# Kernel optimization log

Measured on AMD Instinct MI355X. Metric: run time of the kernel, lower is better.

The kernel has to match this reference:

```python
import jax, jax.numpy as jnp
import numpy as np


def _compute_gradient(f, src, dst, egw):
    # f: [b, c, n] node features; src/dst: [b, e] edge endpoints; egw: [b, e, d]
    # gradient at node src = sum_edges pinvdx * (f[dst] - f[src])
    fT = f.transpose(0, 2, 1)  # b, n, c
    n = fT.shape[1]
    f_dst = jnp.take_along_axis(fT, dst[..., None], axis=1)  # b, e, c
    f_src = jnp.take_along_axis(fT, src[..., None], axis=1)  # b, e, c
    msg = egw[..., :, None] * (f_dst - f_src)[..., None, :]  # b, e, d, c
    b, e, d, c = msg.shape

    def seg(m, s):
        return jax.ops.segment_sum(m.reshape(e, d * c), s, num_segments=n)

    grad = jax.vmap(seg)(msg, src)  # b, n, d*c
    return grad.transpose(0, 2, 1)  # b, d*c, n


def _forward(x, t, nodes, node_weights, edge_gradient_weights, modes, sp_L,
             fc0_w, fc0_b, Wc, Ws, W0, ws_w, ws_b, gws_w, gws_b,
             fc1_w, fc1_b, fc2_w, fc2_b, directed_edges):
    D = nodes.shape[-1]
    # Fourier bases: modes [k,d,w] scaled by sp_L [d,w]
    temp = jnp.einsum('bxd,kdw->bxkw', nodes, modes * sp_L)
    bc, bs = jnp.cos(temp), jnp.sin(temp)
    b0 = jnp.ones(temp[:, :, :1, :].shape, temp.dtype)
    nw = node_weights[:, :, None, :]
    wbc, wbs, wb0 = bc * nw, bs * nw, b0 * nw

    x_value = x[:, :, :D]
    h = jnp.concatenate([x, t], -1) @ fc0_w + fc0_b  # b, n, c
    h = h.transpose(0, 2, 1)  # b, c, n

    src = directed_edges[..., 0]
    dst = directed_edges[..., 1]
    nlayers = ws_w.shape[0]
    for i in range(nlayers):
        # spectral convolution (real Fourier transform on scattered points)
        xc = jnp.einsum('bcx,bxkw->bckw', h, wbc)
        xs = -jnp.einsum('bcx,bxkw->bckw', h, wbs)
        x0 = jnp.einsum('bcx,bxkw->bckw', h, wb0)
        fc_ = jnp.einsum('bikw,iokw->bokw', xc, Wc[i]) - jnp.einsum('bikw,iokw->bokw', xs, Ws[i])
        fs_ = jnp.einsum('bikw,iokw->bokw', xs, Wc[i]) + jnp.einsum('bikw,iokw->bokw', xc, Ws[i])
        f0_ = jnp.einsum('bikw,iokw->bokw', x0, W0[i])
        x1 = (jnp.einsum('bokw,bxkw->box', f0_, b0)
              + 2.0 * jnp.einsum('bokw,bxkw->box', fc_, bc)
              - 2.0 * jnp.einsum('bokw,bxkw->box', fs_, bs))
        # pointwise linear (Conv1d kernel size 1)
        x2 = jnp.einsum('oc,bcx->box', ws_w[i], h) + ws_b[i][None, :, None]
        # gradient operator + softsign + Conv1d
        g = _compute_gradient(h, src, dst, edge_gradient_weights)  # b, d*c, n
        g = g / (1.0 + jnp.abs(g))  # softsign
        x3 = jnp.einsum('oc,bcx->box', gws_w[i], g) + gws_b[i][None, :, None]
        h = x1 + x2 + x3
        if i != nlayers - 1:
            h = jax.nn.gelu(h, approximate=False)

    h = h.transpose(0, 2, 1)  # b, n, c
    h = jax.nn.gelu(h @ fc1_w + fc1_b, approximate=False)
    h = h @ fc2_w + fc2_b
    return x_value + t * h


def setup_inputs() -> dict:
    B, N, E = 2, 20000, 100000
    D, W, K, C, L, FC, OUT = 3, 1, 128, 128, 3, 128, 3
    key = jax.random.key(0)
    k = jax.random.split(key, 16)
    x = jax.random.normal(k[0], (B, N, D), jnp.float32)
    t = jax.random.uniform(k[1], (B, N, 1), jnp.float32)
    node_mask = jnp.ones((B, N, 1), jnp.int32)
    nodes = jax.random.uniform(k[2], (B, N, D), jnp.float32)
    node_weights = jax.random.uniform(k[3], (B, N, W), jnp.float32) / N
    directed_edges = jax.random.randint(k[4], (B, E, 2), 0, N)
    edge_gradient_weights = jax.random.normal(k[5], (B, E, D), jnp.float32)
    modes = jax.random.normal(k[6], (K, D, W), jnp.float32) * (2.0 * np.pi)
    sp_L = jnp.ones((D, W), jnp.float32)
    fc0_w = jax.random.normal(k[7], (D + 1, C), jnp.float32) * 0.1
    fc0_b = jnp.zeros((C,), jnp.float32)
    scale = 1.0 / (C * C)
    Wc = jax.random.uniform(k[8], (L, C, C, K, W), jnp.float32) * scale
    Ws = jax.random.uniform(k[9], (L, C, C, K, W), jnp.float32) * scale
    W0 = jax.random.uniform(k[10], (L, C, C, 1, W), jnp.float32) * scale
    ws_w = jax.random.normal(k[11], (L, C, C), jnp.float32) * 0.05
    ws_b = jnp.zeros((L, C), jnp.float32)
    gws_w = jax.random.normal(k[12], (L, C, D * C), jnp.float32) * 0.05
    gws_b = jnp.zeros((L, C), jnp.float32)
    fc1_w = jax.random.normal(k[13], (C, FC), jnp.float32) * 0.05
    fc1_b = jnp.zeros((FC,), jnp.float32)
    fc2_w = jax.random.normal(k[14], (FC, OUT), jnp.float32) * 0.05
    fc2_b = jnp.zeros((OUT,), jnp.float32)
    return dict(x=x, t=t, node_mask=node_mask, nodes=nodes, node_weights=node_weights,
                directed_edges=directed_edges, edge_gradient_weights=edge_gradient_weights,
                modes=modes, sp_L=sp_L, fc0_w=fc0_w, fc0_b=fc0_b, Wc=Wc, Ws=Ws, W0=W0,
                ws_w=ws_w, ws_b=ws_b, gws_w=gws_w, gws_b=gws_b,
                fc1_w=fc1_w, fc1_b=fc1_b, fc2_w=fc2_w, fc2_b=fc2_b)


def reference(x, t, node_mask, nodes, node_weights, directed_edges, edge_gradient_weights,
              modes, sp_L, fc0_w, fc0_b, Wc, Ws, W0, ws_w, ws_b, gws_w, gws_b,
              fc1_w, fc1_b, fc2_w, fc2_b):
    del node_mask  # unpacked but unused in the original forward
    return _forward(x, t, nodes, node_weights, edge_gradient_weights, modes, sp_L,
                    fc0_w, fc0_b, Wc, Ws, W0, ws_w, ws_b, gws_w, gws_b,
                    fc1_w, fc1_b, fc2_w, fc2_b, directed_edges)
```

## Files before the change

### kernel.cpp

```cpp
#include <hip/hip_runtime.h>
#include <math.h>

#define BB 2
#define NN 20000
#define EE 100000
#define DD 3
#define KK 128
#define CC 128
#define LL 3
#define FCC 128
#define GJ (DD*CC)
#define KR 768
#define NP 20096
#define NCHK 157
#define G1CH 79
#define G1N 256

typedef __attribute__((ext_vector_type(8))) short bf16x8;
typedef __attribute__((ext_vector_type(4))) float f32x4;

__device__ inline unsigned short f2bf(float f) {
  unsigned int u = __float_as_uint(f);
  u += 0x7fffu + ((u >> 16) & 1u);
  return (unsigned short)(u >> 16);
}
__device__ inline float bf2f(unsigned short u) {
  return __uint_as_float(((unsigned int)u) << 16);
}

__device__ float d_nw[BB*NN];
__device__ __align__(16) unsigned short d_stackT[(size_t)BB*NP*KR];
__device__ __align__(16) unsigned short d_bcT[(size_t)BB*KK*NP];
__device__ __align__(16) unsigned short d_bsT[(size_t)BB*KK*NP];
__device__ __align__(16) unsigned short d_hTwT[(size_t)BB*CC*NP];
__device__ __align__(16) float d_hnewT[(size_t)BB*NP*CC];
__device__ __align__(16) float d_uT[(size_t)BB*NP*FCC];
__device__ __align__(16) unsigned short d_Amatb[BB*CC*KR];
__device__ __align__(16) unsigned short d_fc1wb[FCC*CC];
__device__ __align__(16) float d_part[(size_t)BB*G1CH*2*128*128];
__device__ float d_xc[BB*CC*KK];
__device__ float d_xs[BB*CC*KK];
__device__ float d_x0p[BB*NCHK*CC];
__device__ float d_fcv[BB*CC*KK];
__device__ float d_fsv[BB*CC*KK];
__device__ float d_bias[BB*CC];
__device__ int d_cnt[BB*NN];
__device__ int d_cursor[BB*NN];
__device__ int d_off[BB*(NN+1)];
__device__ __align__(16) float4 d_erec[(size_t)BB*EE];

__global__ __launch_bounds__(128) void k_basis(const float* __restrict__ nodes,
                                               const float* __restrict__ nodew,
                                               const float* __restrict__ modes,
                                               const float* __restrict__ spL) {
  int bn = blockIdx.x;
  int k  = threadIdx.x;
  int b = bn / NN, n = bn % NN;
  float x0 = nodes[bn*3+0], x1 = nodes[bn*3+1], x2 = nodes[bn*3+2];
  float tmp = x0*modes[k*3+0]*spL[0] + x1*modes[k*3+1]*spL[1] + x2*modes[k*3+2]*spL[2];
  float cv = cosf(tmp), sv = sinf(tmp);
  size_t row = (size_t)(b*NP + n);
  d_stackT[row*KR + k]       = f2bf(cv);
  d_stackT[row*KR + 128 + k] = f2bf(sv);
  if (k == 0) d_nw[bn] = nodew[bn];
}

__global__ __launch_bounds__(256) void k_basisT() {
  __shared__ unsigned short t1[32][136];
  __shared__ unsigned short t2[32][136];
  int blk = blockIdx.x;
  int nt = blk % 628, b = blk / 628;
  int n0 = nt*32;
  int tid = threadIdx.x;
  int kl = tid & 127, ng = tid >> 7;
  for (int nn = ng; nn < 32; nn += 2) {
    int n = n0 + nn;
    unsigned short cv = 0, sv = 0;
    if (n < NN) {
      const unsigned short* sp = d_stackT + ((size_t)(b*NP + n))*KR;
      cv = sp[kl]; sv = sp[128 + kl];
    }
    t1[nn][kl] = cv;
    t2[nn][kl] = sv;
  }
  __syncthreads();
  int nl = tid & 31, kg = tid >> 5;
  for (int k = kg; k < 128; k += 8) {
    d_bcT[((size_t)(b*KK + k))*NP + n0 + nl] = t1[nl][k];
    d_bsT[((size_t)(b*KK + k))*NP + n0 + nl] = t2[nl][k];
  }
}

__global__ __launch_bounds__(256) void k_csr_zero() {
  int tid = blockIdx.x*256 + threadIdx.x;
  if (tid < BB*NN) { d_cnt[tid] = 0; d_cursor[tid] = 0; }
}

__global__ __launch_bounds__(256) void k_csr_count(const int* __restrict__ edges) {
  int e = blockIdx.x*256 + threadIdx.x;
  if (e >= BB*EE) return;
  int b = e / EE;
  int src = edges[e*2 + 0];
  atomicAdd(&d_cnt[b*NN + src], 1);
}

__global__ __launch_bounds__(1024) void k_csr_scan() {
  int b = blockIdx.x;
  __shared__ int sdata[1024];
  __shared__ int carry_s;
  int tid = threadIdx.x;
  if (tid == 0) carry_s = 0;
  __syncthreads();
  for (int chunk = 0; chunk < 20; ++chunk) {
    int i = chunk*1024 + tid;
    int v = (i < NN) ? d_cnt[b*NN + i] : 0;
    sdata[tid] = v;
    __syncthreads();
    for (int s = 1; s < 1024; s <<= 1) {
      int tv = (tid >= s) ? sdata[tid - s] : 0;
      __syncthreads();
      sdata[tid] += tv;
      __syncthreads();
    }
    int excl = carry_s + sdata[tid] - v;
    if (i < NN) d_off[b*(NN+1) + i] = excl;
    __syncthreads();
    if (tid == 1023) carry_s += sdata[1023];
    __syncthreads();
  }
  if (tid == 0) d_off[b*(NN+1) + NN] = carry_s;
}

__global__ __launch_bounds__(256) void k_csr_scatter(const int* __restrict__ edges,
                                                     const float* __restrict__ egw) {
  int e = blockIdx.x*256 + threadIdx.x;
  if (e >= BB*EE) return;
  int b = e / EE;
  int src = edges[e*2 + 0];
  int dst = edges[e*2 + 1];
  int pos = atomicAdd(&d_cursor[b*NN + src], 1);
  d_erec[(size_t)b*EE + d_off[b*(NN+1) + src] + pos] =
      make_float4(__int_as_float(dst), egw[e*3+0], egw[e*3+1], egw[e*3+2]);
}

__global__ __launch_bounds__(256) void k_h0(const float* __restrict__ x,
                                            const float* __restrict__ t,
                                            const float* __restrict__ w,
                                            const float* __restrict__ bias) {
  int tid = blockIdx.x*256 + threadIdx.x;
  int c = tid & 127;
  int bn = tid >> 7;
  int b = bn / NN, n = bn % NN;
  const float* xv = x + bn*3;
  float acc = bias[c] + xv[0]*w[c] + xv[1]*w[CC+c] + xv[2]*w[2*CC+c]
            + t[bn]*w[3*CC+c];
  size_t row = (size_t)(b*NP + n);
  d_hnewT[row*CC + c] = acc;
  d_stackT[row*KR + 256 + c] = f2bf(acc);
}

__global__ __launch_bounds__(256) void k_hT0() {
  __shared__ unsigned short t[128][136];
  int chunk = blockIdx.x;
  int b = blockIdx.y;
  int n0 = chunk*128;
  int tid = threadIdx.x;
  int cl = tid & 127, ng = tid >> 7;
  for (int nn = ng; nn < 128; nn += 2) {
    int n = n0 + nn;
    unsigned short v = 0;
    if (n < NN) v = f2bf(d_hnewT[((size_t)(b*NP + n))*CC + cl] * d_nw[b*NN + n]);
    t[nn][cl] = v;
  }
  __syncthreads();
  int nl = tid & 31, cg = tid >> 5;
  for (int c = cg; c < 128; c += 8)
    for (int nn2 = 0; nn2 < 128; nn2 += 32)
      d_hTwT[((size_t)(b*CC + c))*NP + n0 + nn2 + nl] = t[nn2 + nl][c];
}

__global__ __launch_bounds__(256) void k_gemm1m() {
  __shared__ unsigned short Bsh[2][128][40];
  int chunk = blockIdx.x;
  int b = blockIdx.y;
  int tid = threadIdx.x, lane = tid & 63, wid = tid >> 6;
  int q = lane >> 4, m = lane & 15;
  f32x4 accC[2][8], accS[2][8];
  #pragma unroll
  for (int i = 0; i < 2; i++)
    #pragma unroll
    for (int j = 0; j < 8; j++) { accC[i][j] = (f32x4){0.f,0.f,0.f,0.f}; accS[i][j] = (f32x4){0.f,0.f,0.f,0.f}; }
  const unsigned short* Ab = d_hTwT + (size_t)b*CC*NP;
  const unsigned short* Bcp = d_bcT + (size_t)b*KK*NP;
  const unsigned short* Bsp = d_bsT + (size_t)b*KK*NP;
  int n0 = chunk*G1N;
  for (int s = 0; s < G1N/32; s++) {
    int nb = n0 + s*32;
    if (nb >= NP) break;
    __syncthreads();
    {
      int arr = tid >> 7, row = tid & 127;
      const unsigned short* src = (arr ? Bsp : Bcp) + (size_t)row*NP + nb;
      unsigned short* dr = &Bsh[arr][row][0];
      *(uint4*)&dr[0]  = *(const uint4*)&src[0];
      *(uint4*)&dr[8]  = *(const uint4*)&src[8];
      *(uint4*)&dr[16] = *(const uint4*)&src[16];
      *(uint4*)&dr[24] = *(const uint4*)&src[24];
    }
    __syncthreads();
    bf16x8 a0 = *(const bf16x8*)(Ab + (size_t)(wid*32 + m)*NP + nb + q*8);
    bf16x8 a1 = *(const bf16x8*)(Ab + (size_t)(wid*32 + 16 + m)*NP + nb + q*8);
    #pragma unroll
    for (int kt = 0; kt < 8; kt++) {
      bf16x8 bcf = *(const bf16x8*)&Bsh[0][kt*16 + m][q*8];
      bf16x8 bsf = *(const bf16x8*)&Bsh[1][kt*16 + m][q*8];
      accC[0][kt] = __builtin_amdgcn_mfma_f32_16x16x32_bf16(a0, bcf, accC[0][kt], 0, 0, 0);
      accC[1][kt] = __builtin_amdgcn_mfma_f32_16x16x32_bf16(a1, bcf, accC[1][kt], 0, 0, 0);
      accS[0][kt] = __builtin_amdgcn_mfma_f32_16x16x32_bf16(a0, bsf, accS[0][kt], 0, 0, 0);
      accS[1][kt] = __builtin_amdgcn_mfma_f32_16x16x32_bf16(a1, bsf, accS[1][kt], 0, 0, 0);
    }
  }
  float* base = d_part + (((size_t)b*G1CH + chunk)*2)*16384;
  #pragma unroll
  for (int mt = 0; mt < 2; mt++)
    #pragma unroll
    for (int kt = 0; kt < 8; kt++)
      #pragma unroll
      for (int r = 0; r < 4; r++) {
        int c = wid*32 + mt*16 + q*4 + r;
        int k = kt*16 + m;
        base[c*128 + k]         =  accC[mt][kt][r];
        base[16384 + c*128 + k] = -accS[mt][kt][r];
      }
}

__global__ __launch_bounds__(256) void k_reduce1() {
  int tid = blockIdx.x*256 + threadIdx.x;
  int k = tid & 127;
  int c = (tid >> 7) & 127;
  int arr = (tid >> 14) & 1;
  int b = tid >> 15;
  const float* p = d_part + (((size_t)b*G1CH)*2 + arr)*16384 + c*128 + k;
  float acc = 0.f;
  for (int ch = 0; ch < G1CH; ch++) acc += p[(size_t)ch*2*16384];
  if (arr == 0) d_xc[(b*CC + c)*KK + k] = acc;
  else          d_xs[(b*CC + c)*KK + k] = acc;
}

__global__ __launch_bounds__(256) void k_x0() {
  int chunk = blockIdx.x;
  int b = blockIdx.y;
  int tid = threadIdx.x;
  int c = tid >> 1, half = tid & 1;
  const unsigned short* p = d_hTwT + ((size_t)(b*CC + c))*NP + chunk*128 + half*64;
  float acc = 0.f;
  #pragma unroll
  for (int i = 0; i < 8; i++) {
    ushort4 v0 = *(const ushort4*)&p[i*8];
    ushort4 v1 = *(const ushort4*)&p[i*8 + 4];
    acc += bf2f(v0.x) + bf2f(v0.y) + bf2f(v0.z) + bf2f(v0.w)
         + bf2f(v1.x) + bf2f(v1.y) + bf2f(v1.z) + bf2f(v1.w);
  }
  __shared__ float red[128][2];
  red[c][half] = acc;
  __syncthreads();
  if (half == 0) d_x0p[(b*NCHK + chunk)*CC + c] = red[c][0] + red[c][1];
}

__global__ __launch_bounds__(128) void k_spec(const float* __restrict__ Wc,
                                              const float* __restrict__ Ws, int l) {
  int b = blockIdx.x >> 7;
  int o = blockIdx.x & 127;
  int k = threadIdx.x;
  const float* wcp = Wc + ((size_t)(l*CC)*CC + o)*KK + k;
  const float* wsp = Ws + ((size_t)(l*CC)*CC + o)*KK + k;
  float fc = 0.f, fs = 0.f;
  for (int i = 0; i < CC; i++) {
    float xcv = d_xc[(b*CC + i)*KK + k];
    float xsv = d_xs[(b*CC + i)*KK + k];
    float wcv = wcp[(size_t)i*CC*KK];
    float wsv = wsp[(size_t)i*CC*KK];
    fc += xcv*wcv - xsv*wsv;
    fs += xsv*wcv + xcv*wsv;
  }
  d_fcv[(b*CC + o)*KK + k] = fc;
  d_fsv[(b*CC + o)*KK + k] = fs;
}

__global__ __launch_bounds__(128) void k_f0(const float* __restrict__ W0,
                                            const float* __restrict__ wsb,
                                            const float* __restrict__ gwsb, int l) {
  int b = blockIdx.x;
  int o = threadIdx.x;
  __shared__ float sx[CC];
  float xv = 0.f;
  for (int p = 0; p < NCHK; p++) xv += d_x0p[(b*NCHK + p)*CC + o];
  sx[o] = xv;
  __syncthreads();
  float acc = 0.f;
  for (int i = 0; i < CC; i++) acc += sx[i]*W0[(l*CC + i)*CC + o];
  d_bias[b*CC + o] = acc + wsb[l*CC + o] + gwsb[l*CC + o];
}

__global__ __launch_bounds__(128) void k_buildAb(const float* __restrict__ wsw,
                                                 const float* __restrict__ gwsw, int l) {
  int bo = blockIdx.x;
  int b = bo >> 7, o = bo & 127;
  int t = threadIdx.x;
  unsigned short* dst = d_Amatb + (size_t)bo*KR;
  dst[t]       = f2bf( 2.f*d_fcv[(size_t)bo*KK + t]);
  dst[128 + t] = f2bf(-2.f*d_fsv[(size_t)bo*KK + t]);
  dst[256 + t] = f2bf(wsw[(l*CC + o)*CC + t]);
  #pragma unroll
  for (int j = 0; j < 3; j++)
    dst[384 + j*128 + t] = f2bf(gwsw[(size_t)(l*CC + o)*GJ + j*128 + t]);
}

__global__ __launch_bounds__(128) void k_fc1w(const float* __restrict__ fc1w) {
  int c = blockIdx.x;
  int o2 = threadIdx.x;
  d_fc1wb[o2*CC + c] = f2bf(fc1w[c*FCC + o2]);
}

__global__ __launch_bounds__(128) void k_grad_csr() {
  int bn = blockIdx.x;
  int b = bn / NN, n = bn % NN;
  int c = threadIdx.x;
  int beg = d_off[b*(NN+1) + n];
  int end = d_off[b*(NN+1) + n + 1];
  const float4* rp = d_erec + (size_t)b*EE;
  const float* hb = d_hnewT + (size_t)b*NP*CC + c;
  float a0 = 0.f, a1 = 0.f, a2 = 0.f;
  float sw0 = 0.f, sw1 = 0.f, sw2 = 0.f;
  int p = beg;
  for (; p + 2 <= end; p += 2) {
    float4 r1 = rp[p], r2 = rp[p+1];
    float f1 = hb[(size_t)__float_as_int(r1.x)*CC];
    float f2 = hb[(size_t)__float_as_int(r2.x)*CC];
    a0 += r1.y*f1 + r2.y*f2;
    a1 += r1.z*f1 + r2.z*f2;
    a2 += r1.w*f1 + r2.w*f2;
    sw0 += r1.y + r2.y; sw1 += r1.z + r2.z; sw2 += r1.w + r2.w;
  }
  if (p < end) {
    float4 r1 = rp[p];
    float f1 = hb[(size_t)__float_as_int(r1.x)*CC];
    a0 += r1.y*f1; a1 += r1.z*f1; a2 += r1.w*f1;
    sw0 += r1.y; sw1 += r1.z; sw2 += r1.w;
  }
  float fs = d_hnewT[((size_t)(b*NP + n))*CC + c];
  a0 -= sw0*fs; a1 -= sw1*fs; a2 -= sw2*fs;
  unsigned short* gp = d_stackT + ((size_t)(b*NP + n))*KR + 384;
  gp[c]        = f2bf(a0/(1.f + fabsf(a0)));
  gp[CC + c]   = f2bf(a1/(1.f + fabsf(a1)));
  gp[2*CC + c] = f2bf(a2/(1.f + fabsf(a2)));
}

__global__ __launch_bounds__(256) void k_mfma(int koff, int K,
                                              const unsigned short* __restrict__ W, size_t wstride,
                                              float* __restrict__ Out,
                                              const float* __restrict__ bias, int bias_stride,
                                              int gelu, int aux) {
  __shared__ unsigned short As[2][64*40];
  __shared__ unsigned short Bs[2][128*40];
  int b = blockIdx.z;
  int n_base = blockIdx.x*64;
  int tid = threadIdx.x;
  int lane = tid & 63, wid = tid >> 6;
  int q = lane >> 4, m = lane & 15;

  f32x4 acc[8];
  #pragma unroll
  for (int j = 0; j < 8; j++) acc[j] = (f32x4){0.f,0.f,0.f,0.f};

  const unsigned short* Wb = W + (size_t)b*wstride;
  const unsigned short* Ab = d_stackT + (size_t)b*NP*KR + koff;

#define STAGE(k0, d) { \
    int rowA = tid >> 2; int e8A = (tid & 3)*8; \
    *(uint4*)&As[d][rowA*40 + e8A] = *(const uint4*)(Ab + (size_t)(n_base + rowA)*KR + (k0) + e8A); \
    _Pragma("unroll") \
    for (int i_ = 0; i_ < 2; i_++) { \
      int idx_ = tid + i_*256; int rowB = idx_ >> 2; int e8B = (idx_ & 3)*8; \
      *(uint4*)&Bs[d][rowB*40 + e8B] = *(const uint4*)(Wb + (size_t)rowB*K + (k0) + e8B); \
    } }

  STAGE(0, 0)
  int cur = 0;
  for (int k0 = 0; k0 < K; k0 += 32) {
    __syncthreads();
    if (k0 + 32 < K) STAGE(k0 + 32, cur ^ 1)
    bf16x8 a = *(const bf16x8*)&As[cur][(wid*16 + m)*40 + q*8];
    #pragma unroll
    for (int ot = 0; ot < 8; ot++) {
      bf16x8 bf = *(const bf16x8*)&Bs[cur][(ot*16 + m)*40 + q*8];
      acc[ot] = __builtin_amdgcn_mfma_f32_16x16x32_bf16(a, bf, acc[ot], 0, 0, 0);
    }
    cur ^= 1;
  }
#undef STAGE

  const float* bp = bias + (size_t)b*bias_stride;
  int nb4 = n_base + wid*16 + q*4;
  float nw4[4];
  #pragma unroll
  for (int r = 0; r < 4; r++)
    nw4[r] = (aux && nb4 + r < NN) ? d_nw[b*NN + nb4 + r] : 0.f;
  #pragma unroll
  for (int ot = 0; ot < 8; ot++) {
    int o = ot*16 + m;
    float bvv = bp[o];
    float vals[4];
    #pragma unroll
    for (int r = 0; r < 4; r++) {
      float v = acc[ot][r] + bvv;
      if (gelu) v = 0.5f*v*(1.f + erff(v*0.70710678118f));
      vals[r] = v;
      Out[((size_t)(b*NP + nb4 + r))*128 + o] = v;
      if (aux && nb4 + r < NN)
        d_stackT[((size_t)(b*NP + nb4 + r))*KR + 256 + o] = f2bf(v);
    }
    if (aux) {
      ushort4 pk;
      pk.x = f2bf(vals[0]*nw4[0]);
      pk.y = f2bf(vals[1]*nw4[1]);
      pk.z = f2bf(vals[2]*nw4[2]);
      pk.w = f2bf(vals[3]*nw4[3]);
      *(ushort4*)&d_hTwT[((size_t)(b*CC + o))*NP + nb4] = pk;
    }
  }
}

__global__ __launch_bounds__(256) void k_out(const float* __restrict__ x,
                                             const float* __restrict__ t,
                                             const float* __restrict__ fc2w,
                                             const float* __restrict__ fc2b,
                                             float* __restrict__ out) {
  int tid = blockIdx.x*256 + threadIdx.x;
  if (tid >= BB*NN) return;
  int b = tid / NN, n = tid % NN;
  const float* up = d_uT + ((size_t)(b*NP + n))*FCC;
  float a0 = fc2b[0], a1 = fc2b[1], a2v = fc2b[2];
  #pragma unroll 4
  for (int o2 = 0; o2 < FCC; o2 += 4) {
    float4 uv = *(const float4*)&up[o2];
    a0  += uv.x*fc2w[(o2+0)*3+0] + uv.y*fc2w[(o2+1)*3+0] + uv.z*fc2w[(o2+2)*3+0] + uv.w*fc2w[(o2+3)*3+0];
    a1  += uv.x*fc2w[(o2+0)*3+1] + uv.y*fc2w[(o2+1)*3+1] + uv.z*fc2w[(o2+2)*3+1] + uv.w*fc2w[(o2+3)*3+1];
    a2v += uv.x*fc2w[(o2+0)*3+2] + uv.y*fc2w[(o2+1)*3+2] + uv.z*fc2w[(o2+2)*3+2] + uv.w*fc2w[(o2+3)*3+2];
  }
  float tv = t[tid];
  out[tid*3 + 0] = x[tid*3 + 0] + tv*a0;
  out[tid*3 + 1] = x[tid*3 + 1] + tv*a1;
  out[tid*3 + 2] = x[tid*3 + 2] + tv*a2v;
}

extern "C" void kernel_launch(void* const* d_in, const int* in_sizes, int n_in,
                              void* d_out, int out_size, void* d_ws, size_t ws_size,
                              hipStream_t stream) {
  const float* x     = (const float*)d_in[0];
  const float* t     = (const float*)d_in[1];
  const float* nodes = (const float*)d_in[3];
  const float* nodew = (const float*)d_in[4];
  const int*   edges = (const int*)d_in[5];
  const float* egw   = (const float*)d_in[6];
  const float* modes = (const float*)d_in[7];
  const float* spL   = (const float*)d_in[8];
  const float* fc0w  = (const float*)d_in[9];
  const float* fc0b  = (const float*)d_in[10];
  const float* Wc    = (const float*)d_in[11];
  const float* Ws    = (const float*)d_in[12];
  const float* W0    = (const float*)d_in[13];
  const float* wsw   = (const float*)d_in[14];
  const float* wsb   = (const float*)d_in[15];
  const float* gwsw  = (const float*)d_in[16];
  const float* gwsb  = (const float*)d_in[17];
  const float* fc1w  = (const float*)d_in[18];
  const float* fc1b  = (const float*)d_in[19];
  const float* fc2w  = (const float*)d_in[20];
  const float* fc2b  = (const float*)d_in[21];
  float* out = (float*)d_out;

  unsigned short* d_Amatb_p; hipGetSymbolAddress((void**)&d_Amatb_p, HIP_SYMBOL(d_Amatb));
  unsigned short* d_fc1wb_p; hipGetSymbolAddress((void**)&d_fc1wb_p, HIP_SYMBOL(d_fc1wb));
  float* d_hnewT_p; hipGetSymbolAddress((void**)&d_hnewT_p, HIP_SYMBOL(d_hnewT));
  float* d_uT_p;    hipGetSymbolAddress((void**)&d_uT_p,    HIP_SYMBOL(d_uT));
  float* d_bias_p;  hipGetSymbolAddress((void**)&d_bias_p,  HIP_SYMBOL(d_bias));

  hipLaunchKernelGGL(k_basis, dim3(BB*NN), dim3(128), 0, stream, nodes, nodew, modes, spL);
  hipLaunchKernelGGL(k_basisT, dim3(628*BB), dim3(256), 0, stream);
  hipLaunchKernelGGL(k_h0, dim3(BB*NN*CC/256), dim3(256), 0, stream, x, t, fc0w, fc0b);
  hipLaunchKernelGGL(k_hT0, dim3(NCHK, BB), dim3(256), 0, stream);
  hipLaunchKernelGGL(k_fc1w, dim3(CC), dim3(FCC), 0, stream, fc1w);
  hipLaunchKernelGGL(k_csr_zero, dim3((BB*NN + 255)/256), dim3(256), 0, stream);
  hipLaunchKernelGGL(k_csr_count, dim3((BB*EE + 255)/256), dim3(256), 0, stream, edges);
  hipLaunchKernelGGL(k_csr_scan, dim3(BB), dim3(1024), 0, stream);
  hipLaunchKernelGGL(k_csr_scatter, dim3((BB*EE + 255)/256), dim3(256), 0, stream, edges, egw);

  for (int l = 0; l < LL; l++) {
    hipLaunchKernelGGL(k_gemm1m, dim3(G1CH, BB), dim3(256), 0, stream);
    hipLaunchKernelGGL(k_reduce1, dim3(256), dim3(256), 0, stream);
    hipLaunchKernelGGL(k_x0, dim3(NCHK, BB), dim3(256), 0, stream);
    hipLaunchKernelGGL(k_spec, dim3(BB*CC), dim3(128), 0, stream, Wc, Ws, l);
    hipLaunchKernelGGL(k_f0, dim3(BB), dim3(CC), 0, stream, W0, wsb, gwsb, l);
    hipLaunchKernelGGL(k_buildAb, dim3(BB*CC), dim3(128), 0, stream, wsw, gwsw, l);
    hipLaunchKernelGGL(k_grad_csr, dim3(BB*NN), dim3(128), 0, stream);
    hipLaunchKernelGGL(k_mfma, dim3(NP/64, 1, BB), dim3(256), 0, stream,
                       0, KR, d_Amatb_p, (size_t)CC*KR, d_hnewT_p, d_bias_p, CC,
                       (l != LL-1) ? 1 : 0, 1);
  }

  hipLaunchKernelGGL(k_mfma, dim3(NP/64, 1, BB), dim3(256), 0, stream,
                     256, CC, d_fc1wb_p, (size_t)0, d_uT_p, fc1b, 0, 1, 0);
  hipLaunchKernelGGL(k_out, dim3((BB*NN + 255)/256), dim3(256), 0, stream, x, t, fc2w, fc2b, out);
}
```

Baseline: 563.5 us.

## Load MFMA operands directly from global memory into registers, dropping LDS staging

```diff
diff --git a/kernel.cpp b/kernel.cpp
--- a/kernel.cpp
+++ b/kernel.cpp
@@ -361,8 +361,6 @@
                                               float* __restrict__ Out,
                                               const float* __restrict__ bias, int bias_stride,
                                               int gelu, int aux) {
-  __shared__ unsigned short As[2][64*40];
-  __shared__ unsigned short Bs[2][128*40];
   int b = blockIdx.z;
   int n_base = blockIdx.x*64;
   int tid = threadIdx.x;
@@ -373,32 +371,34 @@
   #pragma unroll
   for (int j = 0; j < 8; j++) acc[j] = (f32x4){0.f,0.f,0.f,0.f};
 
-  const unsigned short* Wb = W + (size_t)b*wstride;
-  const unsigned short* Ab = d_stackT + (size_t)b*NP*KR + koff;
-
-#define STAGE(k0, d) { \
-    int rowA = tid >> 2; int e8A = (tid & 3)*8; \
-    *(uint4*)&As[d][rowA*40 + e8A] = *(const uint4*)(Ab + (size_t)(n_base + rowA)*KR + (k0) + e8A); \
-    _Pragma("unroll") \
-    for (int i_ = 0; i_ < 2; i_++) { \
-      int idx_ = tid + i_*256; int rowB = idx_ >> 2; int e8B = (idx_ & 3)*8; \
-      *(uint4*)&Bs[d][rowB*40 + e8B] = *(const uint4*)(Wb + (size_t)rowB*K + (k0) + e8B); \
-    } }
-
-  STAGE(0, 0)
-  int cur = 0;
-  for (int k0 = 0; k0 < K; k0 += 32) {
-    __syncthreads();
-    if (k0 + 32 < K) STAGE(k0 + 32, cur ^ 1)
-    bf16x8 a = *(const bf16x8*)&As[cur][(wid*16 + m)*40 + q*8];
-    #pragma unroll
-    for (int ot = 0; ot < 8; ot++) {
-      bf16x8 bf = *(const bf16x8*)&Bs[cur][(ot*16 + m)*40 + q*8];
-      acc[ot] = __builtin_amdgcn_mfma_f32_16x16x32_bf16(a, bf, acc[ot], 0, 0, 0);
-    }
-    cur ^= 1;
-  }
-#undef STAGE
+  const unsigned short* Arow = d_stackT + (size_t)b*NP*KR + koff
+                             + (size_t)(n_base + wid*16 + m)*KR + q*8;
+  const unsigned short* Brow = W + (size_t)b*wstride + (size_t)m*K + q*8;
+
+  bf16x8 aP, bP[8], aQ, bQ[8];
+  aP = *(const bf16x8*)Arow;
+  #pragma unroll
+  for (int ot = 0; ot < 8; ot++) bP[ot] = *(const bf16x8*)(Brow + (size_t)(ot*16)*K);
+
+  int nch = K >> 5;
+  for (int ch = 0; ch < nch; ch += 2) {
+    int k1 = (ch + 1)*32;
+    aQ = *(const bf16x8*)(Arow + k1);
+    #pragma unroll
+    for (int ot = 0; ot < 8; ot++) bQ[ot] = *(const bf16x8*)(Brow + (size_t)(ot*16)*K + k1);
+    #pragma unroll
+    for (int ot = 0; ot < 8; ot++)
+      acc[ot] = __builtin_amdgcn_mfma_f32_16x16x32_bf16(aP, bP[ot], acc[ot], 0, 0, 0);
+    if (ch + 2 < nch) {
+      int k2 = (ch + 2)*32;
+      aP = *(const bf16x8*)(Arow + k2);
+      #pragma unroll
+      for (int ot = 0; ot < 8; ot++) bP[ot] = *(const bf16x8*)(Brow + (size_t)(ot*16)*K + k2);
+    }
+    #pragma unroll
+    for (int ot = 0; ot < 8; ot++)
+      acc[ot] = __builtin_amdgcn_mfma_f32_16x16x32_bf16(aQ, bQ[ot], acc[ot], 0, 0, 0);
+  }
 
   const float* bp = bias + (size_t)b*bias_stride;
   int nb4 = n_base + wid*16 + q*4;
```

New measurement: 710.7 us. 1.26x slower.
